# Kernel tuning notes

Hardware: AMD Instinct MI355X
Metric: run time of the kernel (lower is better)

The kernel has to match this reference:

```python
import jax, jax.numpy as jnp
import numpy as np

N_NODES = 100000
N_EDGES = 1600000
N_GRAPHS = 256
D_IN = 128
D_HID = 128
D_OUT = 7
BN_EPS = 1e-5


def setup_inputs() -> dict:
    key = jax.random.key(0)
    ks = jax.random.split(key, 16)
    def lin(k, fan_in, fan_out):
        # torch.nn.Linear init: U(-1/sqrt(fan_in), 1/sqrt(fan_in)); stored as [in, out]
        bound = 1.0 / np.sqrt(fan_in)
        kw, kb = jax.random.split(k)
        w = jax.random.uniform(kw, (fan_in, fan_out), jnp.float32, -bound, bound)
        b = jax.random.uniform(kb, (fan_out,), jnp.float32, -bound, bound)
        return w, b
    x = jax.random.normal(ks[0], (N_NODES, D_IN), jnp.float32)
    edge_index = jax.random.randint(ks[1], (2, N_EDGES), 0, N_NODES, jnp.int64)
    batch = jnp.sort(jax.random.randint(ks[2], (N_NODES,), 0, N_GRAPHS, jnp.int64))
    w1a, b1a = lin(ks[3], D_IN, D_HID)
    w1b, b1b = lin(ks[4], D_HID, D_HID)
    w2a, b2a = lin(ks[5], D_HID, D_HID)
    w2b, b2b = lin(ks[6], D_HID, D_HID)
    wl, bl = lin(ks[7], D_HID, D_OUT)
    g1 = jnp.ones((D_HID,), jnp.float32); be1 = jnp.zeros((D_HID,), jnp.float32)
    g2 = jnp.ones((D_HID,), jnp.float32); be2 = jnp.zeros((D_HID,), jnp.float32)
    return {"x": x, "w1a": w1a, "b1a": b1a, "w1b": w1b, "b1b": b1b,
            "g1": g1, "be1": be1,
            "w2a": w2a, "b2a": b2a, "w2b": w2b, "b2b": b2b,
            "g2": g2, "be2": be2,
            "wl": wl, "bl": bl,
            "edge_index": edge_index, "batch": batch}


def gin_conv(x, edge_index, wa, ba, wb, bb):
    src, dst = edge_index[0], edge_index[1]
    # sum aggregation of source features at target nodes (eps = 0)
    agg = jax.ops.segment_sum(x[src], dst, num_segments=N_NODES)
    h = x + agg
    h = jnp.maximum(h @ wa + ba, 0.0)
    return h @ wb + bb


def batch_norm(x, gamma, beta):
    mean = jnp.mean(x, axis=0)
    var = jnp.mean(jnp.square(x - mean), axis=0)  # biased, training-mode stats
    return (x - mean) * (gamma / jnp.sqrt(var + BN_EPS)) + beta


def reference(x, w1a, b1a, w1b, b1b, g1, be1,
              w2a, b2a, w2b, b2b, g2, be2,
              wl, bl, edge_index, batch):
    h = gin_conv(x, edge_index, w1a, b1a, w1b, b1b)
    h = jnp.maximum(batch_norm(h, g1, be1), 0.0)
    h = gin_conv(h, edge_index, w2a, b2a, w2b, b2b)
    h = jnp.maximum(batch_norm(h, g2, be2), 0.0)
    # global mean pool over graphs
    sums = jax.ops.segment_sum(h, batch, num_segments=N_GRAPHS)
    cnts = jax.ops.segment_sum(jnp.ones((h.shape[0],), h.dtype), batch, num_segments=N_GRAPHS)
    pooled = sums / jnp.maximum(cnts, 1.0)[:, None]  # [G, D_HID]
    logits = pooled @ wl + bl
    return jax.nn.log_softmax(logits, axis=1)
```

## Files before the change

kernel.cpp:

```cpp
#include <hip/hip_runtime.h>
#include <math.h>

#define NN 100000
#define NE 1600000
#define NG 256
#define D 128
#define EPS 1e-5f
#define MAXDEG 64
#define NBINS 196
#define BINSZ 512
#define BINCAP 12288
#define GRID_BIN 125
#define EPB_A 12800
#define GRID_CAST 6250
#define GRID_TW 32
#define GRID_GEMM 782

typedef __attribute__((ext_vector_type(8))) short s16x8;
typedef __attribute__((ext_vector_type(4))) float f32x4;

__device__ __forceinline__ ushort f2b(float f) {
    uint u = __float_as_uint(f);
    uint r = (u + 0x7fffu + ((u >> 16) & 1u)) >> 16;
    return (ushort)r;
}
__device__ __forceinline__ float blo(uint u) { return __uint_as_float(u << 16); }
__device__ __forceinline__ float bhi(uint u) { return __uint_as_float(u & 0xFFFF0000u); }

#define SWZW(lin) ((lin) ^ ((((lin) >> 8) & 7) << 4))

__global__ __launch_bounds__(256) void prep1(const int* __restrict__ esrc, const int* __restrict__ edst,
                                             uint* __restrict__ binbuf, int* __restrict__ bincnt,
                                             const float* __restrict__ x, ushort* __restrict__ xb,
                                             const float* __restrict__ w1a, const float* __restrict__ w1b,
                                             const float* __restrict__ w2a, const float* __restrict__ w2b,
                                             ushort* __restrict__ Wt) {
    int b = blockIdx.x;
    if (b < GRID_BIN) {
        __shared__ int cnt[NBINS], lbase[NBINS];
        const int ebase = b * EPB_A;
        for (int it = 0; it < 13; ++it) {
            for (int t = threadIdx.x; t < NBINS; t += 256) cnt[t] = 0;
            __syncthreads();
            int e = ebase + it * 1024 + threadIdx.x * 4;
            bool valid = (e < ebase + EPB_A);
            int4 s = make_int4(0, 0, 0, 0), d = make_int4(0, 0, 0, 0);
            if (valid) {
                s = *(const int4*)(esrc + e);
                d = *(const int4*)(edst + e);
            }
            int b0 = d.x >> 9, b1 = d.y >> 9, b2 = d.z >> 9, b3 = d.w >> 9;
            int o0 = 0, o1 = 0, o2 = 0, o3 = 0;
            if (valid) {
                o0 = atomicAdd(&cnt[b0], 1);
                o1 = atomicAdd(&cnt[b1], 1);
                o2 = atomicAdd(&cnt[b2], 1);
                o3 = atomicAdd(&cnt[b3], 1);
            }
            __syncthreads();
            for (int t = threadIdx.x; t < NBINS; t += 256)
                lbase[t] = (cnt[t] > 0) ? atomicAdd(&bincnt[t], cnt[t]) : 0;
            __syncthreads();
            if (valid) {
                uint p0 = (uint)(lbase[b0] + o0), p1 = (uint)(lbase[b1] + o1);
                uint p2 = (uint)(lbase[b2] + o2), p3 = (uint)(lbase[b3] + o3);
                if (p0 < BINCAP) binbuf[b0 * BINCAP + p0] = ((uint)(d.x & 511) << 17) | (uint)s.x;
                if (p1 < BINCAP) binbuf[b1 * BINCAP + p1] = ((uint)(d.y & 511) << 17) | (uint)s.y;
                if (p2 < BINCAP) binbuf[b2 * BINCAP + p2] = ((uint)(d.z & 511) << 17) | (uint)s.z;
                if (p3 < BINCAP) binbuf[b3 * BINCAP + p3] = ((uint)(d.w & 511) << 17) | (uint)s.w;
            }
        }
    } else if (b < GRID_BIN + GRID_CAST) {
        int i = (b - GRID_BIN) * 256 + threadIdx.x;
        if (i * 8 < NN * D) {
            float4 v0 = *(const float4*)(x + i * 8);
            float4 v1 = *(const float4*)(x + i * 8 + 4);
            ushort o[8] = {f2b(v0.x), f2b(v0.y), f2b(v0.z), f2b(v0.w),
                           f2b(v1.x), f2b(v1.y), f2b(v1.z), f2b(v1.w)};
            *(uint4*)(xb + i * 8) = *(uint4*)o;
        }
    } else {
        int by = b - GRID_BIN - GRID_CAST;
        int wsel = by >> 3, bx = by & 7;
        const float* W = (wsel == 0) ? w1a : (wsel == 1) ? w1b : (wsel == 2) ? w2a : w2b;
        ushort* T = Wt + wsel * 16384;
        for (int i = bx * 256 + threadIdx.x; i < 16384; i += 8 * 256) {
            int k = i >> 7, cc = i & 127;
            T[(cc << 7) | k] = f2b(W[i]);
        }
    }
}

__global__ __launch_bounds__(256) void drain(const uint* __restrict__ binbuf, const int* __restrict__ bincnt,
                                             int* __restrict__ deg, int* __restrict__ slots) {
    const int bin = blockIdx.x;
    int n = bincnt[bin]; if (n > BINCAP) n = BINCAP;
    __shared__ int cur[BINSZ];
    cur[threadIdx.x] = 0;
    cur[threadIdx.x + 256] = 0;
    __syncthreads();
    const uint* bp = binbuf + bin * BINCAP;
    const int base = bin << 9;
    int i = threadIdx.x;
    for (; i + 768 < n; i += 1024) {
        uint u0 = bp[i], u1 = bp[i + 256], u2 = bp[i + 512], u3 = bp[i + 768];
        int l0 = u0 >> 17, l1 = u1 >> 17, l2 = u2 >> 17, l3 = u3 >> 17;
        int p0 = atomicAdd(&cur[l0], 1);
        int p1 = atomicAdd(&cur[l1], 1);
        int p2 = atomicAdd(&cur[l2], 1);
        int p3 = atomicAdd(&cur[l3], 1);
        slots[((base + l0) << 6) | (p0 & 63)] = (int)(u0 & 0x1FFFFu);
        slots[((base + l1) << 6) | (p1 & 63)] = (int)(u1 & 0x1FFFFu);
        slots[((base + l2) << 6) | (p2 & 63)] = (int)(u2 & 0x1FFFFu);
        slots[((base + l3) << 6) | (p3 & 63)] = (int)(u3 & 0x1FFFFu);
    }
    for (; i < n; i += 256) {
        uint u0 = bp[i];
        int l0 = u0 >> 17;
        int p0 = atomicAdd(&cur[l0], 1);
        slots[((base + l0) << 6) | (p0 & 63)] = (int)(u0 & 0x1FFFFu);
    }
    __syncthreads();
    int node = base + threadIdx.x;
    if (node < NN) deg[node] = cur[threadIdx.x];
    node += 256;
    if (node < NN) deg[node] = cur[threadIdx.x + 256];
}

template <int FUSE_BN>
__global__ __launch_bounds__(256) void gather_slots(ushort* __restrict__ out, const ushort* __restrict__ feat,
                                                    const int* __restrict__ deg, const int* __restrict__ slots,
                                                    const float* __restrict__ scale, const float* __restrict__ shift) {
    int node = __builtin_amdgcn_readfirstlane(blockIdx.x * 4 + (threadIdx.x >> 6));
    if (node >= NN) return;
    int lane = threadIdx.x & 63;
    int n = deg[node];
    n = (n > MAXDEG) ? MAXDEG : n;
    const int* sl = slots + (node << 6);
    float scx = 1.f, scy = 1.f, shx = 0.f, shy = 0.f;
    if (FUSE_BN) {
        float2 sc = *(const float2*)(scale + lane * 2);
        float2 sh = *(const float2*)(shift + lane * 2);
        scx = sc.x; scy = sc.y; shx = sh.x; shy = sh.y;
    }
    uint ub = *(const uint*)(feat + node * D + lane * 2);
    float axv[8], ayv[8];
#pragma unroll
    for (int j = 0; j < 8; ++j) { axv[j] = 0.f; ayv[j] = 0.f; }
    if (FUSE_BN) {
        axv[0] = fmaxf(fmaf(blo(ub), scx, shx), 0.f);
        ayv[0] = fmaxf(fmaf(bhi(ub), scy, shy), 0.f);
    } else {
        axv[0] = blo(ub); ayv[0] = bhi(ub);
    }
    int e = 0;
    for (; e + 15 < n; e += 16) {
        uint u[16];
#pragma unroll
        for (int j = 0; j < 16; ++j) u[j] = *(const uint*)(feat + sl[e + j] * D + lane * 2);
#pragma unroll
        for (int j = 0; j < 16; ++j) {
            int j8 = j & 7;
            if (FUSE_BN) {
                axv[j8] += fmaxf(fmaf(blo(u[j]), scx, shx), 0.f);
                ayv[j8] += fmaxf(fmaf(bhi(u[j]), scy, shy), 0.f);
            } else {
                axv[j8] += blo(u[j]); ayv[j8] += bhi(u[j]);
            }
        }
    }
    for (; e + 7 < n; e += 8) {
        uint u[8];
#pragma unroll
        for (int j = 0; j < 8; ++j) u[j] = *(const uint*)(feat + sl[e + j] * D + lane * 2);
#pragma unroll
        for (int j = 0; j < 8; ++j) {
            if (FUSE_BN) {
                axv[j] += fmaxf(fmaf(blo(u[j]), scx, shx), 0.f);
                ayv[j] += fmaxf(fmaf(bhi(u[j]), scy, shy), 0.f);
            } else {
                axv[j] += blo(u[j]); ayv[j] += bhi(u[j]);
            }
        }
    }
    for (; e + 3 < n; e += 4) {
        uint u[4];
#pragma unroll
        for (int j = 0; j < 4; ++j) u[j] = *(const uint*)(feat + sl[e + j] * D + lane * 2);
#pragma unroll
        for (int j = 0; j < 4; ++j) {
            if (FUSE_BN) {
                axv[j] += fmaxf(fmaf(blo(u[j]), scx, shx), 0.f);
                ayv[j] += fmaxf(fmaf(bhi(u[j]), scy, shy), 0.f);
            } else {
                axv[j] += blo(u[j]); ayv[j] += bhi(u[j]);
            }
        }
    }
    for (; e < n; ++e) {
        uint u0 = *(const uint*)(feat + sl[e] * D + lane * 2);
        if (FUSE_BN) {
            axv[0] += fmaxf(fmaf(blo(u0), scx, shx), 0.f);
            ayv[0] += fmaxf(fmaf(bhi(u0), scy, shy), 0.f);
        } else {
            axv[0] += blo(u0); ayv[0] += bhi(u0);
        }
    }
    float ax = ((axv[0] + axv[1]) + (axv[2] + axv[3])) + ((axv[4] + axv[5]) + (axv[6] + axv[7]));
    float ay = ((ayv[0] + ayv[1]) + (ayv[2] + ayv[3])) + ((ayv[4] + ayv[5]) + (ayv[6] + ayv[7]));
    uint o = (uint)f2b(ax) | ((uint)f2b(ay) << 16);
    *(uint*)(out + node * D + lane * 2) = o;
}

__global__ __launch_bounds__(512, 4) void gemm_dual(const ushort* __restrict__ G,
                                                    const ushort* __restrict__ Wta, const float* __restrict__ ba,
                                                    const ushort* __restrict__ Wtb, const float* __restrict__ bb,
                                                    ushort* __restrict__ H, float4* __restrict__ stat, int nrows) {
    __shared__ ushort wbuf[16384];
    __shared__ ushort tbuf[16384];
    __shared__ float4 red[8][64];
    char* wb = (char*)wbuf;
    char* tb = (char*)tbuf;

    const int tid = threadIdx.x;
    const int lane = tid & 63;
    const int wave = tid >> 6;
    const int lr = lane & 15;
    const int kg = lane >> 4;
    const int rloc = wave * 16 + lr;
    const int grow = blockIdx.x * 128 + rloc;
    const int growc = (grow > nrows - 1) ? (nrows - 1) : grow;
    const int wrow = lr * 256;
    const int wswz = (lr & 7) << 4;

    const ushort* gp = G + growc * D + kg * 8;
    s16x8 af0 = *(const s16x8*)(gp);
    s16x8 af1 = *(const s16x8*)(gp + 32);
    s16x8 af2 = *(const s16x8*)(gp + 64);
    s16x8 af3 = *(const s16x8*)(gp + 96);

#pragma unroll
    for (int i = 0; i < 4; ++i) {
        int lin = i * 8192 + tid * 16;
        uint4 v = *(const uint4*)((const char*)Wta + lin);
        *(uint4*)(wb + SWZW(lin)) = v;
    }
    __syncthreads();

    f32x4 acc[8];
#pragma unroll
    for (int ct = 0; ct < 8; ++ct) acc[ct] = (f32x4)0.f;

#pragma unroll
    for (int ks = 0; ks < 4; ++ks) {
        s16x8 af = (ks == 0) ? af0 : (ks == 1) ? af1 : (ks == 2) ? af2 : af3;
        const int wofs = (kg * 16 + ks * 64) ^ wswz;
#pragma unroll
        for (int ct = 0; ct < 8; ++ct) {
            s16x8 a = *(const s16x8*)(wb + wrow + ct * 4096 + wofs);
            acc[ct] = __builtin_amdgcn_mfma_f32_16x16x32_bf16(a, af, acc[ct], 0, 0, 0);
        }
    }

#pragma unroll
    for (int ct = 0; ct < 8; ++ct) {
        int k0 = ct * 16 + kg * 4;
        float4 bv = *(const float4*)(ba + k0);
        float o0 = fmaxf(acc[ct][0] + bv.x, 0.f);
        float o1 = fmaxf(acc[ct][1] + bv.y, 0.f);
        float o2 = fmaxf(acc[ct][2] + bv.z, 0.f);
        float o3 = fmaxf(acc[ct][3] + bv.w, 0.f);
        ushort pk[4] = {f2b(o0), f2b(o1), f2b(o2), f2b(o3)};
        int kb = k0 >> 3;
        int off = ((k0 >> 5) << 13) | ((kb & 3) << 11) | ((rloc ^ (kb & 7)) << 4) | ((k0 & 7) << 1);
        *(uint2*)(tb + off) = *(const uint2*)pk;
    }
    __syncthreads();

#pragma unroll
    for (int i = 0; i < 4; ++i) {
        int lin = i * 8192 + tid * 16;
        uint4 v = *(const uint4*)((const char*)Wtb + lin);
        *(uint4*)(wb + SWZW(lin)) = v;
    }
    s16x8 bf[4];
#pragma unroll
    for (int ks = 0; ks < 4; ++ks) {
        int kb = ks * 4 + kg;
        bf[ks] = *(const s16x8*)(tb + ((ks << 13) | (kg << 11) | ((rloc ^ (kb & 7)) << 4)));
    }
    __syncthreads();

#pragma unroll
    for (int ct = 0; ct < 8; ++ct) acc[ct] = (f32x4)0.f;
#pragma unroll
    for (int ks = 0; ks < 4; ++ks) {
        const int wofs = (kg * 16 + ks * 64) ^ wswz;
#pragma unroll
        for (int ct = 0; ct < 8; ++ct) {
            s16x8 a = *(const s16x8*)(wb + wrow + ct * 4096 + wofs);
            acc[ct] = __builtin_amdgcn_mfma_f32_16x16x32_bf16(a, bf[ks], acc[ct], 0, 0, 0);
        }
    }

#pragma unroll
    for (int ct = 0; ct < 8; ++ct) {
        int k0 = ct * 16 + kg * 4;
        float4 bv = *(const float4*)(bb + k0);
        uint2 pk2 = make_uint2(0u, 0u);
        if (grow < nrows) {
            float o0 = acc[ct][0] + bv.x;
            float o1 = acc[ct][1] + bv.y;
            float o2 = acc[ct][2] + bv.z;
            float o3 = acc[ct][3] + bv.w;
            ushort pk[4] = {f2b(o0), f2b(o1), f2b(o2), f2b(o3)};
            pk2 = *(const uint2*)pk;
            *(uint2*)(H + grow * D + k0) = pk2;
        }
        int kb = k0 >> 3;
        int off = ((k0 >> 5) << 13) | ((kb & 3) << 11) | ((rloc ^ (kb & 7)) << 4) | ((k0 & 7) << 1);
        *(uint2*)(tb + off) = pk2;
    }
    __syncthreads();

    {
        int c2 = tid & 63;
        int rg = tid >> 6;
        int k = c2 * 2;
        int kb = k >> 3;
        int base = ((k >> 5) << 13) | ((kb & 3) << 11) | ((k & 7) << 1);
        float s0 = 0.f, q0 = 0.f, s1 = 0.f, q1 = 0.f;
#pragma unroll 4
        for (int i = 0; i < 16; ++i) {
            int row = rg * 16 + i;
            uint u = *(const uint*)(tb + base + ((row ^ (kb & 7)) << 4));
            float lo = blo(u), hi = bhi(u);
            s0 += lo; q0 += lo * lo; s1 += hi; q1 += hi * hi;
        }
        red[rg][c2] = make_float4(s0, q0, s1, q1);
    }
    __syncthreads();
    if (tid < 64) {
        float4 r0 = red[0][tid], r1 = red[1][tid], r2 = red[2][tid], r3 = red[3][tid];
        float4 r4 = red[4][tid], r5 = red[5][tid], r6 = red[6][tid], r7 = red[7][tid];
        float4 o;
        o.x = ((r0.x + r1.x) + (r2.x + r3.x)) + ((r4.x + r5.x) + (r6.x + r7.x));
        o.y = ((r0.y + r1.y) + (r2.y + r3.y)) + ((r4.y + r5.y) + (r6.y + r7.y));
        o.z = ((r0.z + r1.z) + (r2.z + r3.z)) + ((r4.z + r5.z) + (r6.z + r7.z));
        o.w = ((r0.w + r1.w) + (r2.w + r3.w)) + ((r4.w + r5.w) + (r6.w + r7.w));
        stat[blockIdx.x * 64 + tid] = o;
    }
}

__global__ __launch_bounds__(256) void bn_reduce(const float4* __restrict__ stat, int nblk,
                                                 const float* __restrict__ gamma, const float* __restrict__ beta,
                                                 float* __restrict__ scale, float* __restrict__ shift, int nrows) {
    const int f4 = blockIdx.x;
    const int t = threadIdx.x;
    float s0 = 0.f, q0 = 0.f, s1 = 0.f, q1 = 0.f;
    for (int b = t; b < nblk; b += 256) {
        float4 v = stat[b * 64 + f4];
        s0 += v.x; q0 += v.y; s1 += v.z; q1 += v.w;
    }
    __shared__ float4 red[256];
    red[t] = make_float4(s0, q0, s1, q1);
    __syncthreads();
    for (int off = 128; off >= 1; off >>= 1) {
        if (t < off) {
            float4 a = red[t], b = red[t + off];
            red[t] = make_float4(a.x + b.x, a.y + b.y, a.z + b.z, a.w + b.w);
        }
        __syncthreads();
    }
    if (t == 0) {
        float4 v = red[0];
        int f0 = 2 * f4, f1 = 2 * f4 + 1;
        double m0 = (double)v.x / nrows, var0 = (double)v.y / nrows - m0 * m0;
        double m1 = (double)v.z / nrows, var1 = (double)v.w / nrows - m1 * m1;
        float sc0 = gamma[f0] * rsqrtf((float)var0 + EPS);
        float sc1 = gamma[f1] * rsqrtf((float)var1 + EPS);
        scale[f0] = sc0; shift[f0] = beta[f0] - (float)m0 * sc0;
        scale[f1] = sc1; shift[f1] = beta[f1] - (float)m1 * sc1;
    }
}

__global__ __launch_bounds__(256) void pool_partial(const ushort* __restrict__ h, const int* __restrict__ batch,
                                                    const float* __restrict__ scale, const float* __restrict__ shift,
                                                    float* __restrict__ pooled) {
    int wave = threadIdx.x >> 6;
    int lane = threadIdx.x & 63;
    int r0 = blockIdx.x * 256 + wave * 64;
    if (r0 >= NN) return;
    int f2 = lane * 2;
    float2 sc = *(const float2*)(scale + f2);
    float2 sh = *(const float2*)(shift + f2);
    float ax = 0.f, ay = 0.f;
    int cur = -1;
    int rend = r0 + 64; if (rend > NN) rend = NN;
    for (int r = r0; r < rend; ++r) {
        int g = batch[r];
        if (g != cur) {
            if (cur >= 0) {
                atomicAdd(&pooled[cur * D + f2], ax);
                atomicAdd(&pooled[cur * D + f2 + 1], ay);
            }
            cur = g; ax = 0.f; ay = 0.f;
        }
        uint u = *(const uint*)(h + r * D + f2);
        ax += fmaxf(fmaf(blo(u), sc.x, sh.x), 0.f);
        ay += fmaxf(fmaf(bhi(u), sc.y, sh.y), 0.f);
    }
    if (cur >= 0) {
        atomicAdd(&pooled[cur * D + f2], ax);
        atomicAdd(&pooled[cur * D + f2 + 1], ay);
    }
}

__device__ __forceinline__ int lower_bound_i(const int* a, int n, int v) {
    int lo = 0, hi = n;
    while (lo < hi) {
        int m = (lo + hi) >> 1;
        if (a[m] < v) lo = m + 1; else hi = m;
    }
    return lo;
}

__global__ __launch_bounds__(256) void head(const float* __restrict__ pooled, const int* __restrict__ batch,
                                            const float* __restrict__ wl, const float* __restrict__ bl,
                                            float* __restrict__ out) {
    int g = blockIdx.x * 256 + threadIdx.x;
    if (g >= NG) return;
    int lo = lower_bound_i(batch, NN, g);
    int hi = lower_bound_i(batch, NN, g + 1);
    float inv = 1.f / fmaxf((float)(hi - lo), 1.f);
    float logits[7];
#pragma unroll
    for (int c = 0; c < 7; ++c) logits[c] = bl[c];
    for (int k = 0; k < D; ++k) {
        float p = pooled[g * D + k] * inv;
#pragma unroll
        for (int c = 0; c < 7; ++c) logits[c] = fmaf(p, wl[k * 7 + c], logits[c]);
    }
    float m = logits[0];
#pragma unroll
    for (int c = 1; c < 7; ++c) m = fmaxf(m, logits[c]);
    float s = 0.f;
#pragma unroll
    for (int c = 0; c < 7; ++c) s += expf(logits[c] - m);
    float lse = m + logf(s);
#pragma unroll
    for (int c = 0; c < 7; ++c) out[g * 7 + c] = logits[c] - lse;
}

extern "C" void kernel_launch(void* const* d_in, const int* in_sizes, int n_in,
                              void* d_out, int out_size, void* d_ws, size_t ws_size,
                              hipStream_t stream) {
    const float* x   = (const float*)d_in[0];
    const float* w1a = (const float*)d_in[1];
    const float* b1a = (const float*)d_in[2];
    const float* w1b = (const float*)d_in[3];
    const float* b1b = (const float*)d_in[4];
    const float* g1  = (const float*)d_in[5];
    const float* be1 = (const float*)d_in[6];
    const float* w2a = (const float*)d_in[7];
    const float* b2a = (const float*)d_in[8];
    const float* w2b = (const float*)d_in[9];
    const float* b2b = (const float*)d_in[10];
    const float* g2  = (const float*)d_in[11];
    const float* be2 = (const float*)d_in[12];
    const float* wl  = (const float*)d_in[13];
    const float* bl  = (const float*)d_in[14];
    const int* ei    = (const int*)d_in[15];
    const int* batch = (const int*)d_in[16];
    float* out = (float*)d_out;

    const int* esrc = ei;
    const int* edst = ei + NE;

    char* ws = (char*)d_ws;
    ushort* B0 = (ushort*)(ws);
    ushort* B1 = (ushort*)(ws + 25600000);
    ushort* B2 = (ushort*)(ws + 51200000);
    uint* binbuf = (uint*)(ws + 25600000);
    int* slots   = (int*)(ws + 76800000);
    int* deg     = (int*)(ws + 102400000);
    int* bincnt  = (int*)(ws + 102800000);
    float* pooled = (float*)(ws + 102801024);
    float* scale1 = (float*)(ws + 102932096);
    float* shift1 = scale1 + 128;
    float* scale2 = shift1 + 128;
    float* shift2 = scale2 + 128;
    ushort* Wt    = (ushort*)(ws + 102934144);
    float4* stat  = (float4*)(ws + 103065216);
    ushort* Wt1a = Wt, *Wt1b = Wt + 16384, *Wt2a = Wt + 32768, *Wt2b = Wt + 49152;

    const int grid_prep = GRID_BIN + GRID_CAST + GRID_TW;
    const int grid_stat = (NN + 255) / 256;
    const int grid_gath = (NN + 3) / 4;

    hipMemsetAsync(bincnt, 0, 132096, stream);

    prep1<<<grid_prep, 256, 0, stream>>>(esrc, edst, binbuf, bincnt, x, B0, w1a, w1b, w2a, w2b, Wt);
    drain<<<NBINS, 256, 0, stream>>>(binbuf, bincnt, deg, slots);

    gather_slots<0><<<grid_gath, 256, 0, stream>>>(B1, B0, deg, slots, nullptr, nullptr);
    gemm_dual<<<GRID_GEMM, 512, 0, stream>>>(B1, Wt1a, b1a, Wt1b, b1b, B2, stat, NN);
    bn_reduce<<<64, 256, 0, stream>>>(stat, GRID_GEMM, g1, be1, scale1, shift1, NN);

    gather_slots<1><<<grid_gath, 256, 0, stream>>>(B0, B2, deg, slots, scale1, shift1);
    gemm_dual<<<GRID_GEMM, 512, 0, stream>>>(B0, Wt2a, b2a, Wt2b, b2b, B1, stat, NN);
    bn_reduce<<<64, 256, 0, stream>>>(stat, GRID_GEMM, g2, be2, scale2, shift2, NN);

    pool_partial<<<grid_stat, 256, 0, stream>>>(B1, batch, scale2, shift2, pooled);
    head<<<1, 256, 0, stream>>>(pooled, batch, wl, bl, out);
}
```

Baseline: 290.0 us.

## Widen edge binning and pooling grids, vectorize gather accumulation as float2

Edge binning now uses twice as many blocks, each handling half as many edges (7 iterations instead of 13), and the pooling kernel gives each wave 16 rows instead of 64, so both phases expose more parallelism. The gather kernel's accumulators are rewritten as two-wide float vectors so the compiler can emit packed FP32 add, FMA and max instructions. The trade-off is more atomics in pooling and per-block overhead in binning, while the gather change only touches ALU work in what is likely a memory-bound loop.

```diff
diff --git a/kernel.cpp b/kernel.cpp
--- a/kernel.cpp
+++ b/kernel.cpp
@@ -10,14 +10,15 @@
 #define NBINS 196
 #define BINSZ 512
 #define BINCAP 12288
-#define GRID_BIN 125
-#define EPB_A 12800
+#define GRID_BIN 250
+#define EPB_A 6400
 #define GRID_CAST 6250
 #define GRID_TW 32
 #define GRID_GEMM 782
 
 typedef __attribute__((ext_vector_type(8))) short s16x8;
 typedef __attribute__((ext_vector_type(4))) float f32x4;
+typedef __attribute__((ext_vector_type(2))) float f32x2;
 
 __device__ __forceinline__ ushort f2b(float f) {
     uint u = __float_as_uint(f);
@@ -26,6 +27,9 @@
 }
 __device__ __forceinline__ float blo(uint u) { return __uint_as_float(u << 16); }
 __device__ __forceinline__ float bhi(uint u) { return __uint_as_float(u & 0xFFFF0000u); }
+__device__ __forceinline__ f32x2 unpk2(uint u) {
+    f32x2 v; v.x = blo(u); v.y = bhi(u); return v;
+}
 
 #define SWZW(lin) ((lin) ^ ((((lin) >> 8) & 7) << 4))
 
@@ -39,7 +43,7 @@
     if (b < GRID_BIN) {
         __shared__ int cnt[NBINS], lbase[NBINS];
         const int ebase = b * EPB_A;
-        for (int it = 0; it < 13; ++it) {
+        for (int it = 0; it < 7; ++it) {
             for (int t = threadIdx.x; t < NBINS; t += 256) cnt[t] = 0;
             __syncthreads();
             int e = ebase + it * 1024 + threadIdx.x * 4;
@@ -137,21 +141,24 @@
     int n = deg[node];
     n = (n > MAXDEG) ? MAXDEG : n;
     const int* sl = slots + (node << 6);
-    float scx = 1.f, scy = 1.f, shx = 0.f, shy = 0.f;
+    f32x2 sc2 = (f32x2)1.f, sh2 = (f32x2)0.f;
     if (FUSE_BN) {
         float2 sc = *(const float2*)(scale + lane * 2);
         float2 sh = *(const float2*)(shift + lane * 2);
-        scx = sc.x; scy = sc.y; shx = sh.x; shy = sh.y;
+        sc2.x = sc.x; sc2.y = sc.y; sh2.x = sh.x; sh2.y = sh.y;
     }
     uint ub = *(const uint*)(feat + node * D + lane * 2);
-    float axv[8], ayv[8];
-#pragma unroll
-    for (int j = 0; j < 8; ++j) { axv[j] = 0.f; ayv[j] = 0.f; }
-    if (FUSE_BN) {
-        axv[0] = fmaxf(fmaf(blo(ub), scx, shx), 0.f);
-        ayv[0] = fmaxf(fmaf(bhi(ub), scy, shy), 0.f);
-    } else {
-        axv[0] = blo(ub); ayv[0] = bhi(ub);
+    f32x2 acc[8];
+#pragma unroll
+    for (int j = 0; j < 8; ++j) acc[j] = (f32x2)0.f;
+    {
+        f32x2 v = unpk2(ub);
+        if (FUSE_BN) {
+            f32x2 t = v * sc2 + sh2;
+            acc[0] = __builtin_elementwise_max(t, (f32x2)0.f);
+        } else {
+            acc[0] = v;
+        }
     }
     int e = 0;
     for (; e + 15 < n; e += 16) {
@@ -160,12 +167,12 @@
         for (int j = 0; j < 16; ++j) u[j] = *(const uint*)(feat + sl[e + j] * D + lane * 2);
 #pragma unroll
         for (int j = 0; j < 16; ++j) {
-            int j8 = j & 7;
+            f32x2 v = unpk2(u[j]);
             if (FUSE_BN) {
-                axv[j8] += fmaxf(fmaf(blo(u[j]), scx, shx), 0.f);
-                ayv[j8] += fmaxf(fmaf(bhi(u[j]), scy, shy), 0.f);
+                f32x2 t = v * sc2 + sh2;
+                acc[j & 7] += __builtin_elementwise_max(t, (f32x2)0.f);
             } else {
-                axv[j8] += blo(u[j]); ayv[j8] += bhi(u[j]);
+                acc[j & 7] += v;
             }
         }
     }
@@ -175,11 +182,12 @@
         for (int j = 0; j < 8; ++j) u[j] = *(const uint*)(feat + sl[e + j] * D + lane * 2);
 #pragma unroll
         for (int j = 0; j < 8; ++j) {
+            f32x2 v = unpk2(u[j]);
             if (FUSE_BN) {
-                axv[j] += fmaxf(fmaf(blo(u[j]), scx, shx), 0.f);
-                ayv[j] += fmaxf(fmaf(bhi(u[j]), scy, shy), 0.f);
+                f32x2 t = v * sc2 + sh2;
+                acc[j] += __builtin_elementwise_max(t, (f32x2)0.f);
             } else {
-                axv[j] += blo(u[j]); ayv[j] += bhi(u[j]);
+                acc[j] += v;
             }
         }
     }
@@ -189,26 +197,26 @@
         for (int j = 0; j < 4; ++j) u[j] = *(const uint*)(feat + sl[e + j] * D + lane * 2);
 #pragma unroll
         for (int j = 0; j < 4; ++j) {
+            f32x2 v = unpk2(u[j]);
             if (FUSE_BN) {
-                axv[j] += fmaxf(fmaf(blo(u[j]), scx, shx), 0.f);
-                ayv[j] += fmaxf(fmaf(bhi(u[j]), scy, shy), 0.f);
+                f32x2 t = v * sc2 + sh2;
+                acc[j] += __builtin_elementwise_max(t, (f32x2)0.f);
             } else {
-                axv[j] += blo(u[j]); ayv[j] += bhi(u[j]);
+                acc[j] += v;
             }
         }
     }
     for (; e < n; ++e) {
-        uint u0 = *(const uint*)(feat + sl[e] * D + lane * 2);
+        f32x2 v = unpk2(*(const uint*)(feat + sl[e] * D + lane * 2));
         if (FUSE_BN) {
-            axv[0] += fmaxf(fmaf(blo(u0), scx, shx), 0.f);
-            ayv[0] += fmaxf(fmaf(bhi(u0), scy, shy), 0.f);
+            f32x2 t = v * sc2 + sh2;
+            acc[0] += __builtin_elementwise_max(t, (f32x2)0.f);
         } else {
-            axv[0] += blo(u0); ayv[0] += bhi(u0);
-        }
-    }
-    float ax = ((axv[0] + axv[1]) + (axv[2] + axv[3])) + ((axv[4] + axv[5]) + (axv[6] + axv[7]));
-    float ay = ((ayv[0] + ayv[1]) + (ayv[2] + ayv[3])) + ((ayv[4] + ayv[5]) + (ayv[6] + ayv[7]));
-    uint o = (uint)f2b(ax) | ((uint)f2b(ay) << 16);
+            acc[0] += v;
+        }
+    }
+    f32x2 s = ((acc[0] + acc[1]) + (acc[2] + acc[3])) + ((acc[4] + acc[5]) + (acc[6] + acc[7]));
+    uint o = (uint)f2b(s.x) | ((uint)f2b(s.y) << 16);
     *(uint*)(out + node * D + lane * 2) = o;
 }
 
@@ -389,14 +397,14 @@
                                                     float* __restrict__ pooled) {
     int wave = threadIdx.x >> 6;
     int lane = threadIdx.x & 63;
-    int r0 = blockIdx.x * 256 + wave * 64;
+    int r0 = blockIdx.x * 64 + wave * 16;
     if (r0 >= NN) return;
     int f2 = lane * 2;
     float2 sc = *(const float2*)(scale + f2);
     float2 sh = *(const float2*)(shift + f2);
     float ax = 0.f, ay = 0.f;
     int cur = -1;
-    int rend = r0 + 64; if (rend > NN) rend = NN;
+    int rend = r0 + 16; if (rend > NN) rend = NN;
     for (int r = r0; r < rend; ++r) {
         int g = batch[r];
         if (g != cur) {
@@ -495,7 +503,7 @@
     ushort* Wt1a = Wt, *Wt1b = Wt + 16384, *Wt2a = Wt + 32768, *Wt2b = Wt + 49152;
 
     const int grid_prep = GRID_BIN + GRID_CAST + GRID_TW;
-    const int grid_stat = (NN + 255) / 256;
+    const int grid_pool = (NN + 63) / 64;
     const int grid_gath = (NN + 3) / 4;
 
     hipMemsetAsync(bincnt, 0, 132096, stream);
@@ -511,6 +519,6 @@
     gemm_dual<<<GRID_GEMM, 512, 0, stream>>>(B0, Wt2a, b2a, Wt2b, b2b, B1, stat, NN);
     bn_reduce<<<64, 256, 0, stream>>>(stat, GRID_GEMM, g2, be2, scale2, shift2, NN);
 
-    pool_partial<<<grid_stat, 256, 0, stream>>>(B1, batch, scale2, shift2, pooled);
+    pool_partial<<<grid_pool, 256, 0, stream>>>(B1, batch, scale2, shift2, pooled);
     head<<<1, 256, 0, stream>>>(pooled, batch, wl, bl, out);
 }
```

New measurement: 288.5 us. No clear change (-0.5%).
